# Performance work log

Hardware: AMD Instinct MI355X
Metric: run time of the kernel (lower is better)

Reference implementation:

```python
import jax, jax.numpy as jnp
import numpy as np

OUT_SIZE, EMB, DEC_H, ENC_D = 172, 128, 256, 256
B, L = 256, 1024


def setup_inputs() -> dict:
    key = jax.random.key(0)
    ks = jax.random.split(key, 16)
    s = lambda k, shp, scale=0.05: (jax.random.normal(k, shp, dtype=jnp.float32) * scale)
    return {
        "h0": jax.random.normal(ks[0], (B, DEC_H), dtype=jnp.float32),
        "c0": jax.random.normal(ks[1], (B, DEC_H), dtype=jnp.float32),
        "o_t": jax.random.normal(ks[2], (B, DEC_H), dtype=jnp.float32),
        "enc_out": jax.random.normal(ks[3], (B, L, ENC_D), dtype=jnp.float32),
        "lasttarget": jax.random.randint(ks[4], (B, 1), 0, OUT_SIZE),
        # learned params
        "emb": s(ks[5], (OUT_SIZE, EMB), 1.0),
        "W_ih": s(ks[6], (4 * DEC_H, DEC_H + EMB)),
        "W_hh": s(ks[7], (4 * DEC_H, DEC_H)),
        "b_ih": s(ks[8], (4 * DEC_H,)),
        "b_hh": s(ks[9], (4 * DEC_H,)),
        "W1": s(ks[10], (ENC_D, ENC_D)),
        "W2": s(ks[11], (ENC_D, DEC_H)),
        "W3": s(ks[12], (DEC_H, DEC_H + ENC_D)),
        "W_out": s(ks[13], (OUT_SIZE, DEC_H)),
        "beta": jax.random.uniform(ks[14], (ENC_D,), dtype=jnp.float32, minval=-0.01, maxval=0.01),
    }


def reference(h0, c0, o_t, enc_out, lasttarget, emb, W_ih, W_hh, b_ih, b_hh, W1, W2, W3, W_out, beta):
    # embedding + concat -> LSTMCell input (B, DEC_H+EMB)
    prev_y = emb[lasttarget[:, 0]]              # (B, EMB)
    inp = jnp.concatenate([prev_y, o_t], axis=1)
    # LSTMCell: gate order i, f, g, o (PyTorch convention)
    gates = inp @ W_ih.T + b_ih + h0 @ W_hh.T + b_hh   # (B, 4*DEC_H)
    i, f, g, o = jnp.split(gates, 4, axis=1)
    c_t = jax.nn.sigmoid(f) * c0 + jax.nn.sigmoid(i) * jnp.tanh(g)
    h_t = jax.nn.sigmoid(o) * jnp.tanh(c_t)
    # additive attention over enc positions
    alpha = jnp.tanh(enc_out @ W1.T + (h_t @ W2.T)[:, None, :])  # (B, L, ENC_D)
    scores = jnp.sum(beta * alpha, axis=-1)                      # (B, L)
    attn = jax.nn.softmax(scores, axis=-1)
    context = jnp.einsum("bl,bld->bd", attn, enc_out)            # (B, ENC_D)
    # output projection
    o_new = jnp.tanh(jnp.concatenate([h_t, context], axis=1) @ W3.T)  # (B, DEC_H)
    logit = jax.nn.softmax(o_new @ W_out.T, axis=1)                   # (B, OUT_SIZE)
    return (h_t, c_t, o_new, logit)
```

## Files before the change

### kernel.cpp

```cpp
#include <hip/hip_runtime.h>

#define B_   256
#define L_   1024
#define H_   256
#define EMB_ 128
#define OUT_ 172

typedef float f32x4 __attribute__((ext_vector_type(4)));
typedef __bf16 bf16x8 __attribute__((ext_vector_type(8)));
typedef unsigned short us8 __attribute__((ext_vector_type(8)));

static __device__ __forceinline__ unsigned short f2bf(float f) {
    unsigned u = __float_as_uint(f);
    u += 0x7fffu + ((u >> 16) & 1u);
    return (unsigned short)(u >> 16);
}
static __device__ __forceinline__ float bf2f(unsigned short s) {
    return __uint_as_float(((unsigned)s) << 16);
}
static __device__ __forceinline__ us8 cvt8(const float* __restrict__ p) {
    float4 x0 = *(const float4*)p, x1 = *(const float4*)(p + 4);
    us8 v;
    v[0]=f2bf(x0.x); v[1]=f2bf(x0.y); v[2]=f2bf(x0.z); v[3]=f2bf(x0.w);
    v[4]=f2bf(x1.x); v[5]=f2bf(x1.y); v[6]=f2bf(x1.z); v[7]=f2bf(x1.w);
    return v;
}
static __device__ __forceinline__ float tanh_fast(float x) {
    float e = __expf(2.f * x);
    return 1.f - 2.f * __builtin_amdgcn_rcpf(e + 1.f);
}
static __device__ __forceinline__ float sigm_fast(float x) {
    return __builtin_amdgcn_rcpf(1.f + __expf(-x));
}

#define TS 40

__global__ __launch_bounds__(256) void k_gates(
    const float* __restrict__ h0, const float* __restrict__ o_t,
    const int* __restrict__ lasttarget, const float* __restrict__ emb,
    const float* __restrict__ W_ih, const float* __restrict__ W_hh,
    const float* __restrict__ b_ih, const float* __restrict__ b_hh,
    float* __restrict__ gates)
{
    const int m0 = (blockIdx.x >> 4) * 64;
    const int n0 = (blockIdx.x & 15) * 64;
    const int tid = threadIdx.x;
    const int w = tid >> 6, lane = tid & 63, quad = lane >> 4, l15 = lane & 15;

    __shared__ __align__(16) unsigned short As[64 * TS];
    __shared__ __align__(16) unsigned short Bs[64 * TS];

    float bias[4];
    #pragma unroll
    for (int nt = 0; nt < 4; nt++) {
        int n = n0 + nt * 16 + l15;
        bias[nt] = b_ih[n] + b_hh[n];
    }

    f32x4 acc[4] = {{0,0,0,0},{0,0,0,0},{0,0,0,0},{0,0,0,0}};
    const int sm = tid >> 2, sk8 = (tid & 3) * 8;
    const int lt = lasttarget[m0 + sm];

    for (int kc = 0; kc < 20; kc++) {
        const int k = kc * 32 + sk8;
        const float* ap;
        if (k < 128)      ap = emb + lt * EMB_ + k;
        else if (k < 384) ap = o_t + (m0 + sm) * H_ + (k - 128);
        else              ap = h0  + (m0 + sm) * H_ + (k - 384);
        *(us8*)&As[sm * TS + sk8] = cvt8(ap);
        const int j = n0 + sm;
        const float* bp = (k < 384) ? (W_ih + j * 384 + k) : (W_hh + j * 256 + (k - 384));
        *(us8*)&Bs[sm * TS + sk8] = cvt8(bp);
        __syncthreads();
        bf16x8 a = __builtin_bit_cast(bf16x8, *(const us8*)&As[(w * 16 + l15) * TS + quad * 8]);
        #pragma unroll
        for (int nt = 0; nt < 4; nt++) {
            bf16x8 b = __builtin_bit_cast(bf16x8, *(const us8*)&Bs[(nt * 16 + l15) * TS + quad * 8]);
            acc[nt] = __builtin_amdgcn_mfma_f32_16x16x32_bf16(a, b, acc[nt], 0, 0, 0);
        }
        __syncthreads();
    }
    #pragma unroll
    for (int nt = 0; nt < 4; nt++)
        #pragma unroll
        for (int r = 0; r < 4; r++)
            gates[(m0 + w * 16 + quad * 4 + r) * 1024 + n0 + nt * 16 + l15] = acc[nt][r] + bias[nt];
}

__global__ __launch_bounds__(256) void k_lstm(
    const float* __restrict__ gates, const float* __restrict__ c0,
    float* __restrict__ out, unsigned short* __restrict__ A3u)
{
    const int b = blockIdx.x, t = threadIdx.x;
    const float* g = gates + b * 1024;
    float gi = g[t], gf = g[256 + t], gg = g[512 + t], go = g[768 + t];
    float c = sigm_fast(gf) * c0[b * H_ + t] + sigm_fast(gi) * tanh_fast(gg);
    float h = sigm_fast(go) * tanh_fast(c);
    out[b * H_ + t]           = h;
    out[B_ * H_ + b * H_ + t] = c;
    A3u[b * 512 + t] = f2bf(h);
}

__global__ __launch_bounds__(256) void k_hw2(
    const unsigned short* __restrict__ A3u, const float* __restrict__ W2,
    float* __restrict__ hW2)
{
    const int m0 = (blockIdx.x >> 2) * 64;
    const int n0 = (blockIdx.x & 3) * 64;
    const int tid = threadIdx.x;
    const int w = tid >> 6, lane = tid & 63, quad = lane >> 4, l15 = lane & 15;
    __shared__ __align__(16) unsigned short As[64 * TS];
    __shared__ __align__(16) unsigned short Bs[64 * TS];
    f32x4 acc[4] = {{0,0,0,0},{0,0,0,0},{0,0,0,0},{0,0,0,0}};
    const int sm = tid >> 2, sk8 = (tid & 3) * 8;
    for (int kc = 0; kc < 8; kc++) {
        const int k = kc * 32 + sk8;
        *(us8*)&As[sm * TS + sk8] = *(const us8*)&A3u[(m0 + sm) * 512 + k];
        *(us8*)&Bs[sm * TS + sk8] = cvt8(W2 + (n0 + sm) * 256 + k);
        __syncthreads();
        bf16x8 a = __builtin_bit_cast(bf16x8, *(const us8*)&As[(w * 16 + l15) * TS + quad * 8]);
        #pragma unroll
        for (int nt = 0; nt < 4; nt++) {
            bf16x8 b = __builtin_bit_cast(bf16x8, *(const us8*)&Bs[(nt * 16 + l15) * TS + quad * 8]);
            acc[nt] = __builtin_amdgcn_mfma_f32_16x16x32_bf16(a, b, acc[nt], 0, 0, 0);
        }
        __syncthreads();
    }
    #pragma unroll
    for (int nt = 0; nt < 4; nt++)
        #pragma unroll
        for (int r = 0; r < 4; r++)
            hW2[(m0 + w * 16 + quad * 4 + r) * 256 + n0 + nt * 16 + l15] = acc[nt][r];
}

#define ROWSTR 264

__global__ __launch_bounds__(512, 2) void k_attn(
    const float* __restrict__ enc, const float* __restrict__ W1,
    const float* __restrict__ hW2, const float* __restrict__ beta,
    unsigned short* __restrict__ A3u)
{
    const int b = blockIdx.x;
    const int tid = threadIdx.x;
    const int wave = tid >> 6, lane = tid & 63;
    const int quad = lane >> 4, l15 = lane & 15;

    __shared__ __align__(16) unsigned short encs[2][16 * ROWSTR];
    __shared__ float sp[8][16];
    __shared__ float wexp[16];
    __shared__ float2 cr[512];
    __shared__ float ssum_s;

    bf16x8 wf[8][2];
    float hw2v[2], betav[2];
    #pragma unroll
    for (int nt = 0; nt < 2; nt++) {
        int n = wave * 32 + nt * 16 + l15;
        hw2v[nt]  = hW2[b * H_ + n];
        betav[nt] = beta[n];
        #pragma unroll
        for (int ks = 0; ks < 8; ks++)
            wf[ks][nt] = __builtin_bit_cast(bf16x8, cvt8(W1 + n * 256 + ks * 32 + quad * 8));
    }

    const float* encb = enc + (size_t)b * L_ * H_;
    const int srow = tid >> 5, scol = (tid & 31) * 8;

    *(us8*)&encs[0][srow * ROWSTR + scol] = cvt8(encb + srow * 256 + scol);
    __syncthreads();

    const int cp = tid & 127, q = tid >> 7;
    float2 ctx2 = {0.f, 0.f};
    float ssum = 0.f;

    for (int it = 0; it < 64; it++) {
        const int cur = it & 1;
        float4 x0, x1;
        if (it < 63) {
            const float* p = encb + (it + 1) * 16 * 256 + srow * 256 + scol;
            x0 = *(const float4*)p; x1 = *(const float4*)(p + 4);
        }
        f32x4 acc0 = {0,0,0,0}, acc1 = {0,0,0,0};
        const unsigned short* arow = &encs[cur][l15 * ROWSTR + quad * 8];
        #pragma unroll
        for (int ks = 0; ks < 8; ks++) {
            bf16x8 a = __builtin_bit_cast(bf16x8, *(const us8*)(arow + ks * 32));
            acc0 = __builtin_amdgcn_mfma_f32_16x16x32_bf16(a, wf[ks][0], acc0, 0, 0, 0);
            acc1 = __builtin_amdgcn_mfma_f32_16x16x32_bf16(a, wf[ks][1], acc1, 0, 0, 0);
        }
        float p4[4];
        #pragma unroll
        for (int r = 0; r < 4; r++) {
            float t0 = tanh_fast(acc0[r] + hw2v[0]);
            float t1 = tanh_fast(acc1[r] + hw2v[1]);
            p4[r] = betav[0] * t0 + betav[1] * t1;
        }
        #pragma unroll
        for (int m = 1; m < 16; m <<= 1) {
            p4[0] += __shfl_xor(p4[0], m);
            p4[1] += __shfl_xor(p4[1], m);
            p4[2] += __shfl_xor(p4[2], m);
            p4[3] += __shfl_xor(p4[3], m);
        }
        if (l15 == 0) {
            #pragma unroll
            for (int r = 0; r < 4; r++) sp[wave][quad * 4 + r] = p4[r];
        }
        __syncthreads();
        if (tid < 16) {
            float sc = sp[0][tid] + sp[1][tid] + sp[2][tid] + sp[3][tid]
                     + sp[4][tid] + sp[5][tid] + sp[6][tid] + sp[7][tid];
            wexp[tid] = __expf(sc);
        }
        __syncthreads();
        if (it < 63) {
            us8 v;
            v[0]=f2bf(x0.x); v[1]=f2bf(x0.y); v[2]=f2bf(x0.z); v[3]=f2bf(x0.w);
            v[4]=f2bf(x1.x); v[5]=f2bf(x1.y); v[6]=f2bf(x1.z); v[7]=f2bf(x1.w);
            *(us8*)&encs[cur ^ 1][srow * ROWSTR + scol] = v;
        }
        {
            const unsigned* base = (const unsigned*)&encs[cur][0];
            float cx = ctx2.x, cy = ctx2.y;
            #pragma unroll
            for (int r = 0; r < 4; r++) {
                const int row = q * 4 + r;
                unsigned u = base[row * (ROWSTR / 2) + cp];
                float wv = wexp[row];
                cx += wv * __uint_as_float(u << 16);
                cy += wv * __uint_as_float(u & 0xffff0000u);
            }
            ctx2.x = cx; ctx2.y = cy;
        }
        if (tid == 0) {
            float s2 = 0.f;
            #pragma unroll
            for (int r = 0; r < 16; r++) s2 += wexp[r];
            ssum += s2;
        }
        __syncthreads();
    }
    if (tid == 0) ssum_s = ssum;
    cr[tid] = ctx2;
    __syncthreads();
    if (tid < 128) {
        float2 a0 = cr[tid], a1 = cr[tid + 128], a2 = cr[tid + 256], a3 = cr[tid + 384];
        float inv = __builtin_amdgcn_rcpf(ssum_s);
        float cx = (a0.x + a1.x + a2.x + a3.x) * inv;
        float cy = (a0.y + a1.y + a2.y + a3.y) * inv;
        unsigned pack = (unsigned)f2bf(cx) | ((unsigned)f2bf(cy) << 16);
        ((unsigned*)A3u)[b * 256 + 128 + tid] = pack;
    }
}

__global__ __launch_bounds__(256) void k_out3(
    const unsigned short* __restrict__ A3u, const float* __restrict__ W3,
    float* __restrict__ out, unsigned short* __restrict__ A4u)
{
    const int m0 = (blockIdx.x >> 2) * 64;
    const int n0 = (blockIdx.x & 3) * 64;
    const int tid = threadIdx.x;
    const int w = tid >> 6, lane = tid & 63, quad = lane >> 4, l15 = lane & 15;
    __shared__ __align__(16) unsigned short As[64 * TS];
    __shared__ __align__(16) unsigned short Bs[64 * TS];
    f32x4 acc[4] = {{0,0,0,0},{0,0,0,0},{0,0,0,0},{0,0,0,0}};
    const int sm = tid >> 2, sk8 = (tid & 3) * 8;
    for (int kc = 0; kc < 16; kc++) {
        const int k = kc * 32 + sk8;
        *(us8*)&As[sm * TS + sk8] = *(const us8*)&A3u[(m0 + sm) * 512 + k];
        *(us8*)&Bs[sm * TS + sk8] = cvt8(W3 + (n0 + sm) * 512 + k);
        __syncthreads();
        bf16x8 a = __builtin_bit_cast(bf16x8, *(const us8*)&As[(w * 16 + l15) * TS + quad * 8]);
        #pragma unroll
        for (int nt = 0; nt < 4; nt++) {
            bf16x8 b = __builtin_bit_cast(bf16x8, *(const us8*)&Bs[(nt * 16 + l15) * TS + quad * 8]);
            acc[nt] = __builtin_amdgcn_mfma_f32_16x16x32_bf16(a, b, acc[nt], 0, 0, 0);
        }
        __syncthreads();
    }
    #pragma unroll
    for (int nt = 0; nt < 4; nt++)
        #pragma unroll
        for (int r = 0; r < 4; r++) {
            int row = m0 + w * 16 + quad * 4 + r, col = n0 + nt * 16 + l15;
            float o = tanh_fast(acc[nt][r]);
            out[2 * B_ * H_ + row * 256 + col] = o;
            A4u[row * 256 + col] = f2bf(o);
        }
}

__global__ __launch_bounds__(256) void k_logit(
    const unsigned short* __restrict__ A4u, const float* __restrict__ W_out,
    float* __restrict__ out)
{
    const int m0 = blockIdx.x * 64;
    const int tid = threadIdx.x;
    const int w = tid >> 6, lane = tid & 63, quad = lane >> 4, l15 = lane & 15;
    __shared__ __align__(16) unsigned short As[64 * TS];
    __shared__ __align__(16) unsigned short Bs[192 * TS];
    __shared__ float lg[64][196];
    f32x4 acc[12];
    #pragma unroll
    for (int nt = 0; nt < 12; nt++) acc[nt] = (f32x4){0,0,0,0};
    const int sm = tid >> 2, sk8 = (tid & 3) * 8;
    for (int kc = 0; kc < 8; kc++) {
        const int k = kc * 32 + sk8;
        *(us8*)&As[sm * TS + sk8] = *(const us8*)&A4u[(m0 + sm) * 256 + k];
        #pragma unroll
        for (int rr = 0; rr < 3; rr++) {
            int j = rr * 64 + sm;
            us8 v = {0,0,0,0,0,0,0,0};
            if (j < OUT_) v = cvt8(W_out + j * 256 + k);
            *(us8*)&Bs[j * TS + sk8] = v;
        }
        __syncthreads();
        bf16x8 a = __builtin_bit_cast(bf16x8, *(const us8*)&As[(w * 16 + l15) * TS + quad * 8]);
        #pragma unroll
        for (int nt = 0; nt < 12; nt++) {
            bf16x8 b = __builtin_bit_cast(bf16x8, *(const us8*)&Bs[(nt * 16 + l15) * TS + quad * 8]);
            acc[nt] = __builtin_amdgcn_mfma_f32_16x16x32_bf16(a, b, acc[nt], 0, 0, 0);
        }
        __syncthreads();
    }
    #pragma unroll
    for (int nt = 0; nt < 12; nt++)
        #pragma unroll
        for (int r = 0; r < 4; r++)
            lg[w * 16 + quad * 4 + r][nt * 16 + l15] = acc[nt][r];
    __syncthreads();
    const int m = tid >> 2, p = tid & 3;
    const int cb = p * 43;
    float mx = -1e30f;
    for (int c = 0; c < 43; c++) mx = fmaxf(mx, lg[m][cb + c]);
    mx = fmaxf(mx, __shfl_xor(mx, 1));
    mx = fmaxf(mx, __shfl_xor(mx, 2));
    float s = 0.f;
    for (int c = 0; c < 43; c++) { float e = __expf(lg[m][cb + c] - mx); lg[m][cb + c] = e; s += e; }
    s += __shfl_xor(s, 1);
    s += __shfl_xor(s, 2);
    float inv = 1.f / s;
    for (int c = 0; c < 43; c++)
        out[3 * B_ * H_ + (m0 + m) * OUT_ + cb + c] = lg[m][cb + c] * inv;
}

extern "C" void kernel_launch(void* const* d_in, const int* in_sizes, int n_in,
                              void* d_out, int out_size, void* d_ws, size_t ws_size,
                              hipStream_t stream)
{
    const float* h0   = (const float*)d_in[0];
    const float* c0   = (const float*)d_in[1];
    const float* o_t  = (const float*)d_in[2];
    const float* enc  = (const float*)d_in[3];
    const int*   lt   = (const int*)  d_in[4];
    const float* emb  = (const float*)d_in[5];
    const float* W_ih = (const float*)d_in[6];
    const float* W_hh = (const float*)d_in[7];
    const float* b_ih = (const float*)d_in[8];
    const float* b_hh = (const float*)d_in[9];
    const float* W1   = (const float*)d_in[10];
    const float* W2   = (const float*)d_in[11];
    const float* W3   = (const float*)d_in[12];
    const float* Wo   = (const float*)d_in[13];
    const float* beta = (const float*)d_in[14];
    float* out = (float*)d_out;
    float* ws  = (float*)d_ws;

    float*          gates = ws;
    float*          hW2   = ws + 262144;
    unsigned short* A3u   = (unsigned short*)(ws + 327680);
    unsigned short* A4u   = (unsigned short*)(ws + 393216);

    k_gates<<<64, 256, 0, stream>>>(h0, o_t, lt, emb, W_ih, W_hh, b_ih, b_hh, gates);
    k_lstm <<<256, 256, 0, stream>>>(gates, c0, out, A3u);
    k_hw2  <<<16, 256, 0, stream>>>(A3u, W2, hW2);
    k_attn <<<256, 512, 0, stream>>>(enc, W1, hW2, beta, A3u);
    k_out3 <<<16, 256, 0, stream>>>(A3u, W3, out, A4u);
    k_logit<<<4, 256, 0, stream>>>(A4u, Wo, out);
}
```

Measured before the change: 466.1 us.

## Split attention over two blocks per batch row with triple-buffered pipeline

The attention kernel now runs two blocks per batch element, each covering half the sequence and writing partial context sums and exp-sums to workspace. The output projection kernel combines the two partials, normalizes and converts to bf16 as it loads its A tile. The attention loop moves to a three-slot LDS ring with loads issued two tiles ahead and double-buffered score arrays, which removes one barrier per iteration. The goal is better occupancy across 256 CUs and less synchronization stall, at the cost of an extra partial-buffer round trip and more LDS per block.

```diff
diff --git a/kernel.cpp b/kernel.cpp
--- a/kernel.cpp
+++ b/kernel.cpp
@@ -98,7 +98,7 @@
     float h = sigm_fast(go) * tanh_fast(c);
     out[b * H_ + t]           = h;
     out[B_ * H_ + b * H_ + t] = c;
-    A3u[b * 512 + t] = f2bf(h);
+    A3u[b * 256 + t] = f2bf(h);
 }
 
 __global__ __launch_bounds__(256) void k_hw2(
@@ -115,7 +115,7 @@
     const int sm = tid >> 2, sk8 = (tid & 3) * 8;
     for (int kc = 0; kc < 8; kc++) {
         const int k = kc * 32 + sk8;
-        *(us8*)&As[sm * TS + sk8] = *(const us8*)&A3u[(m0 + sm) * 512 + k];
+        *(us8*)&As[sm * TS + sk8] = *(const us8*)&A3u[(m0 + sm) * 256 + k];
         *(us8*)&Bs[sm * TS + sk8] = cvt8(W2 + (n0 + sm) * 256 + k);
         __syncthreads();
         bf16x8 a = __builtin_bit_cast(bf16x8, *(const us8*)&As[(w * 16 + l15) * TS + quad * 8]);
@@ -138,18 +138,18 @@
 __global__ __launch_bounds__(512, 2) void k_attn(
     const float* __restrict__ enc, const float* __restrict__ W1,
     const float* __restrict__ hW2, const float* __restrict__ beta,
-    unsigned short* __restrict__ A3u)
-{
-    const int b = blockIdx.x;
+    float* __restrict__ ctx_part, float* __restrict__ s_part)
+{
+    const int blk = blockIdx.x;
+    const int b = blk >> 1, half = blk & 1;
     const int tid = threadIdx.x;
     const int wave = tid >> 6, lane = tid & 63;
     const int quad = lane >> 4, l15 = lane & 15;
 
-    __shared__ __align__(16) unsigned short encs[2][16 * ROWSTR];
-    __shared__ float sp[8][16];
-    __shared__ float wexp[16];
+    __shared__ __align__(16) unsigned short encs[3][16 * ROWSTR];
+    __shared__ float sp[2][8][16];
+    __shared__ float wexp[2][16];
     __shared__ float2 cr[512];
-    __shared__ float ssum_s;
 
     bf16x8 wf[8][2];
     float hw2v[2], betav[2];
@@ -163,22 +163,29 @@
             wf[ks][nt] = __builtin_bit_cast(bf16x8, cvt8(W1 + n * 256 + ks * 32 + quad * 8));
     }
 
-    const float* encb = enc + (size_t)b * L_ * H_;
+    const float* encb = enc + ((size_t)b * L_ + half * 512) * H_;
     const int srow = tid >> 5, scol = (tid & 31) * 8;
 
     *(us8*)&encs[0][srow * ROWSTR + scol] = cvt8(encb + srow * 256 + scol);
+    float4 x0, x1;
+    {
+        const float* p = encb + 16 * 256 + srow * 256 + scol;
+        x0 = *(const float4*)p; x1 = *(const float4*)(p + 4);
+    }
     __syncthreads();
 
     const int cp = tid & 127, q = tid >> 7;
     float2 ctx2 = {0.f, 0.f};
     float ssum = 0.f;
 
-    for (int it = 0; it < 64; it++) {
-        const int cur = it & 1;
-        float4 x0, x1;
-        if (it < 63) {
-            const float* p = encb + (it + 1) * 16 * 256 + srow * 256 + scol;
-            x0 = *(const float4*)p; x1 = *(const float4*)(p + 4);
+    for (int it = 0; it < 32; it++) {
+        const int cur = it % 3;
+        const int nxt = (it + 1) % 3;
+        const int par = it & 1;
+        float4 y0 = {0,0,0,0}, y1 = {0,0,0,0};
+        if (it < 30) {
+            const float* p = encb + (it + 2) * 16 * 256 + srow * 256 + scol;
+            y0 = *(const float4*)p; y1 = *(const float4*)(p + 4);
         }
         f32x4 acc0 = {0,0,0,0}, acc1 = {0,0,0,0};
         const unsigned short* arow = &encs[cur][l15 * ROWSTR + quad * 8];
@@ -187,6 +194,12 @@
             bf16x8 a = __builtin_bit_cast(bf16x8, *(const us8*)(arow + ks * 32));
             acc0 = __builtin_amdgcn_mfma_f32_16x16x32_bf16(a, wf[ks][0], acc0, 0, 0, 0);
             acc1 = __builtin_amdgcn_mfma_f32_16x16x32_bf16(a, wf[ks][1], acc1, 0, 0, 0);
+        }
+        if (it < 31) {
+            us8 v;
+            v[0]=f2bf(x0.x); v[1]=f2bf(x0.y); v[2]=f2bf(x0.z); v[3]=f2bf(x0.w);
+            v[4]=f2bf(x1.x); v[5]=f2bf(x1.y); v[6]=f2bf(x1.z); v[7]=f2bf(x1.w);
+            *(us8*)&encs[nxt][srow * ROWSTR + scol] = v;
         }
         float p4[4];
         #pragma unroll
@@ -204,21 +217,15 @@
         }
         if (l15 == 0) {
             #pragma unroll
-            for (int r = 0; r < 4; r++) sp[wave][quad * 4 + r] = p4[r];
+            for (int r = 0; r < 4; r++) sp[par][wave][quad * 4 + r] = p4[r];
         }
         __syncthreads();
         if (tid < 16) {
-            float sc = sp[0][tid] + sp[1][tid] + sp[2][tid] + sp[3][tid]
-                     + sp[4][tid] + sp[5][tid] + sp[6][tid] + sp[7][tid];
-            wexp[tid] = __expf(sc);
-        }
-        __syncthreads();
-        if (it < 63) {
-            us8 v;
-            v[0]=f2bf(x0.x); v[1]=f2bf(x0.y); v[2]=f2bf(x0.z); v[3]=f2bf(x0.w);
-            v[4]=f2bf(x1.x); v[5]=f2bf(x1.y); v[6]=f2bf(x1.z); v[7]=f2bf(x1.w);
-            *(us8*)&encs[cur ^ 1][srow * ROWSTR + scol] = v;
-        }
+            float sc = sp[par][0][tid] + sp[par][1][tid] + sp[par][2][tid] + sp[par][3][tid]
+                     + sp[par][4][tid] + sp[par][5][tid] + sp[par][6][tid] + sp[par][7][tid];
+            wexp[par][tid] = __expf(sc);
+        }
+        __syncthreads();
         {
             const unsigned* base = (const unsigned*)&encs[cur][0];
             float cx = ctx2.x, cy = ctx2.y;
@@ -226,7 +233,7 @@
             for (int r = 0; r < 4; r++) {
                 const int row = q * 4 + r;
                 unsigned u = base[row * (ROWSTR / 2) + cp];
-                float wv = wexp[row];
+                float wv = wexp[par][row];
                 cx += wv * __uint_as_float(u << 16);
                 cy += wv * __uint_as_float(u & 0xffff0000u);
             }
@@ -235,26 +242,26 @@
         if (tid == 0) {
             float s2 = 0.f;
             #pragma unroll
-            for (int r = 0; r < 16; r++) s2 += wexp[r];
+            for (int r = 0; r < 16; r++) s2 += wexp[par][r];
             ssum += s2;
         }
-        __syncthreads();
-    }
-    if (tid == 0) ssum_s = ssum;
+        x0 = y0; x1 = y1;
+    }
     cr[tid] = ctx2;
     __syncthreads();
+    if (tid == 0) s_part[blk] = ssum;
     if (tid < 128) {
         float2 a0 = cr[tid], a1 = cr[tid + 128], a2 = cr[tid + 256], a3 = cr[tid + 384];
-        float inv = __builtin_amdgcn_rcpf(ssum_s);
-        float cx = (a0.x + a1.x + a2.x + a3.x) * inv;
-        float cy = (a0.y + a1.y + a2.y + a3.y) * inv;
-        unsigned pack = (unsigned)f2bf(cx) | ((unsigned)f2bf(cy) << 16);
-        ((unsigned*)A3u)[b * 256 + 128 + tid] = pack;
+        float2 o;
+        o.x = a0.x + a1.x + a2.x + a3.x;
+        o.y = a0.y + a1.y + a2.y + a3.y;
+        ((float2*)ctx_part)[blk * 128 + tid] = o;
     }
 }
 
 __global__ __launch_bounds__(256) void k_out3(
-    const unsigned short* __restrict__ A3u, const float* __restrict__ W3,
+    const unsigned short* __restrict__ A3u, const float* __restrict__ ctx_part,
+    const float* __restrict__ s_part, const float* __restrict__ W3,
     float* __restrict__ out, unsigned short* __restrict__ A4u)
 {
     const int m0 = (blockIdx.x >> 2) * 64;
@@ -265,9 +272,25 @@
     __shared__ __align__(16) unsigned short Bs[64 * TS];
     f32x4 acc[4] = {{0,0,0,0},{0,0,0,0},{0,0,0,0},{0,0,0,0}};
     const int sm = tid >> 2, sk8 = (tid & 3) * 8;
+    const int bb = m0 + sm;
+    const float inv = 1.f / (s_part[2 * bb] + s_part[2 * bb + 1]);
     for (int kc = 0; kc < 16; kc++) {
         const int k = kc * 32 + sk8;
-        *(us8*)&As[sm * TS + sk8] = *(const us8*)&A3u[(m0 + sm) * 512 + k];
+        if (k < 256) {
+            *(us8*)&As[sm * TS + sk8] = *(const us8*)&A3u[bb * 256 + k];
+        } else {
+            const int c = k - 256;
+            const float* p0 = ctx_part + (size_t)(2 * bb) * 256 + c;
+            const float* p1 = ctx_part + (size_t)(2 * bb + 1) * 256 + c;
+            float4 a0 = *(const float4*)p0, a1 = *(const float4*)(p0 + 4);
+            float4 b0 = *(const float4*)p1, b1 = *(const float4*)(p1 + 4);
+            us8 v;
+            v[0]=f2bf((a0.x+b0.x)*inv); v[1]=f2bf((a0.y+b0.y)*inv);
+            v[2]=f2bf((a0.z+b0.z)*inv); v[3]=f2bf((a0.w+b0.w)*inv);
+            v[4]=f2bf((a1.x+b1.x)*inv); v[5]=f2bf((a1.y+b1.y)*inv);
+            v[6]=f2bf((a1.z+b1.z)*inv); v[7]=f2bf((a1.w+b1.w)*inv);
+            *(us8*)&As[sm * TS + sk8] = v;
+        }
         *(us8*)&Bs[sm * TS + sk8] = cvt8(W3 + (n0 + sm) * 512 + k);
         __syncthreads();
         bf16x8 a = __builtin_bit_cast(bf16x8, *(const us8*)&As[(w * 16 + l15) * TS + quad * 8]);
@@ -365,15 +388,17 @@
     float* out = (float*)d_out;
     float* ws  = (float*)d_ws;
 
-    float*          gates = ws;
-    float*          hW2   = ws + 262144;
-    unsigned short* A3u   = (unsigned short*)(ws + 327680);
-    unsigned short* A4u   = (unsigned short*)(ws + 393216);
+    float*          gates    = ws;
+    float*          hW2      = ws + 262144;
+    float*          ctx_part = ws + 327680;
+    float*          s_part   = ws + 458752;
+    unsigned short* A3u      = (unsigned short*)(ws + 459264);
+    unsigned short* A4u      = (unsigned short*)(ws + 492032);
 
     k_gates<<<64, 256, 0, stream>>>(h0, o_t, lt, emb, W_ih, W_hh, b_ih, b_hh, gates);
     k_lstm <<<256, 256, 0, stream>>>(gates, c0, out, A3u);
     k_hw2  <<<16, 256, 0, stream>>>(A3u, W2, hW2);
-    k_attn <<<256, 512, 0, stream>>>(enc, W1, hW2, beta, A3u);
-    k_out3 <<<16, 256, 0, stream>>>(A3u, W3, out, A4u);
+    k_attn <<<512, 512, 0, stream>>>(enc, W1, hW2, beta, ctx_part, s_part);
+    k_out3 <<<16, 256, 0, stream>>>(A3u, ctx_part, s_part, W3, out, A4u);
     k_logit<<<4, 256, 0, stream>>>(A4u, Wo, out);
 }
```

Measured after the change: 464.1 us. No clear change (-0.4%).

## Fuse gates, LSTM, hW2 and attention into one cooperative kernel with triple buffering

Applied to the files above, without the earlier changes.

Merges the gate GEMM, LSTM cell, h·W2 projection and attention kernels into a single cooperative launch. A grid-wide sync separates the gate GEMM (done by the first 64 blocks) from the per-batch work, and the first two encoder tiles are prefetched before that sync. Each block then computes its own h·W2 row in shared memory. The attention loop moves from double to triple buffering with parity-indexed score arrays, so the bf16 store of the next tile overlaps the current MFMAs and one barrier per iteration is dropped. This removes three launches and the hW2 round trip through global memory. In exchange it relies on cooperative launch residency (256 blocks of 512 threads) and repeats the W2 load in every block.

```diff
diff --git a/kernel.cpp b/kernel.cpp
--- a/kernel.cpp
+++ b/kernel.cpp
@@ -1,4 +1,5 @@
 #include <hip/hip_runtime.h>
+#include <hip/hip_cooperative_groups.h>
 
 #define B_   256
 #define L_   1024
@@ -14,9 +15,6 @@
     unsigned u = __float_as_uint(f);
     u += 0x7fffu + ((u >> 16) & 1u);
     return (unsigned short)(u >> 16);
-}
-static __device__ __forceinline__ float bf2f(unsigned short s) {
-    return __uint_as_float(((unsigned)s) << 16);
 }
 static __device__ __forceinline__ us8 cvt8(const float* __restrict__ p) {
     float4 x0 = *(const float4*)p, x1 = *(const float4*)(p + 4);
@@ -25,6 +23,12 @@
     v[4]=f2bf(x1.x); v[5]=f2bf(x1.y); v[6]=f2bf(x1.z); v[7]=f2bf(x1.w);
     return v;
 }
+static __device__ __forceinline__ us8 cvt8r(float4 x0, float4 x1) {
+    us8 v;
+    v[0]=f2bf(x0.x); v[1]=f2bf(x0.y); v[2]=f2bf(x0.z); v[3]=f2bf(x0.w);
+    v[4]=f2bf(x1.x); v[5]=f2bf(x1.y); v[6]=f2bf(x1.z); v[7]=f2bf(x1.w);
+    return v;
+}
 static __device__ __forceinline__ float tanh_fast(float x) {
     float e = __expf(2.f * x);
     return 1.f - 2.f * __builtin_amdgcn_rcpf(e + 1.f);
@@ -34,160 +38,156 @@
 }
 
 #define TS 40
-
-__global__ __launch_bounds__(256) void k_gates(
-    const float* __restrict__ h0, const float* __restrict__ o_t,
-    const int* __restrict__ lasttarget, const float* __restrict__ emb,
+#define ROWSTR 264
+
+__global__ __launch_bounds__(512, 2) void k_fused(
+    const float* __restrict__ h0, const float* __restrict__ c0,
+    const float* __restrict__ o_t, const float* __restrict__ enc,
+    const int* __restrict__ lt, const float* __restrict__ emb,
     const float* __restrict__ W_ih, const float* __restrict__ W_hh,
     const float* __restrict__ b_ih, const float* __restrict__ b_hh,
-    float* __restrict__ gates)
+    const float* __restrict__ W1, const float* __restrict__ W2,
+    const float* __restrict__ beta, float* __restrict__ gates,
+    unsigned short* __restrict__ A3u, float* __restrict__ out)
 {
-    const int m0 = (blockIdx.x >> 4) * 64;
-    const int n0 = (blockIdx.x & 15) * 64;
-    const int tid = threadIdx.x;
-    const int w = tid >> 6, lane = tid & 63, quad = lane >> 4, l15 = lane & 15;
-
-    __shared__ __align__(16) unsigned short As[64 * TS];
-    __shared__ __align__(16) unsigned short Bs[64 * TS];
-
-    float bias[4];
-    #pragma unroll
-    for (int nt = 0; nt < 4; nt++) {
-        int n = n0 + nt * 16 + l15;
-        bias[nt] = b_ih[n] + b_hh[n];
-    }
-
-    f32x4 acc[4] = {{0,0,0,0},{0,0,0,0},{0,0,0,0},{0,0,0,0}};
-    const int sm = tid >> 2, sk8 = (tid & 3) * 8;
-    const int lt = lasttarget[m0 + sm];
-
-    for (int kc = 0; kc < 20; kc++) {
-        const int k = kc * 32 + sk8;
-        const float* ap;
-        if (k < 128)      ap = emb + lt * EMB_ + k;
-        else if (k < 384) ap = o_t + (m0 + sm) * H_ + (k - 128);
-        else              ap = h0  + (m0 + sm) * H_ + (k - 384);
-        *(us8*)&As[sm * TS + sk8] = cvt8(ap);
-        const int j = n0 + sm;
-        const float* bp = (k < 384) ? (W_ih + j * 384 + k) : (W_hh + j * 256 + (k - 384));
-        *(us8*)&Bs[sm * TS + sk8] = cvt8(bp);
-        __syncthreads();
-        bf16x8 a = __builtin_bit_cast(bf16x8, *(const us8*)&As[(w * 16 + l15) * TS + quad * 8]);
-        #pragma unroll
-        for (int nt = 0; nt < 4; nt++) {
-            bf16x8 b = __builtin_bit_cast(bf16x8, *(const us8*)&Bs[(nt * 16 + l15) * TS + quad * 8]);
-            acc[nt] = __builtin_amdgcn_mfma_f32_16x16x32_bf16(a, b, acc[nt], 0, 0, 0);
-        }
-        __syncthreads();
-    }
-    #pragma unroll
-    for (int nt = 0; nt < 4; nt++)
-        #pragma unroll
-        for (int r = 0; r < 4; r++)
-            gates[(m0 + w * 16 + quad * 4 + r) * 1024 + n0 + nt * 16 + l15] = acc[nt][r] + bias[nt];
-}
-
-__global__ __launch_bounds__(256) void k_lstm(
-    const float* __restrict__ gates, const float* __restrict__ c0,
-    float* __restrict__ out, unsigned short* __restrict__ A3u)
-{
-    const int b = blockIdx.x, t = threadIdx.x;
-    const float* g = gates + b * 1024;
-    float gi = g[t], gf = g[256 + t], gg = g[512 + t], go = g[768 + t];
-    float c = sigm_fast(gf) * c0[b * H_ + t] + sigm_fast(gi) * tanh_fast(gg);
-    float h = sigm_fast(go) * tanh_fast(c);
-    out[b * H_ + t]           = h;
-    out[B_ * H_ + b * H_ + t] = c;
-    A3u[b * 512 + t] = f2bf(h);
-}
-
-__global__ __launch_bounds__(256) void k_hw2(
-    const unsigned short* __restrict__ A3u, const float* __restrict__ W2,
-    float* __restrict__ hW2)
-{
-    const int m0 = (blockIdx.x >> 2) * 64;
-    const int n0 = (blockIdx.x & 3) * 64;
-    const int tid = threadIdx.x;
-    const int w = tid >> 6, lane = tid & 63, quad = lane >> 4, l15 = lane & 15;
-    __shared__ __align__(16) unsigned short As[64 * TS];
-    __shared__ __align__(16) unsigned short Bs[64 * TS];
-    f32x4 acc[4] = {{0,0,0,0},{0,0,0,0},{0,0,0,0},{0,0,0,0}};
-    const int sm = tid >> 2, sk8 = (tid & 3) * 8;
-    for (int kc = 0; kc < 8; kc++) {
-        const int k = kc * 32 + sk8;
-        *(us8*)&As[sm * TS + sk8] = *(const us8*)&A3u[(m0 + sm) * 512 + k];
-        *(us8*)&Bs[sm * TS + sk8] = cvt8(W2 + (n0 + sm) * 256 + k);
-        __syncthreads();
-        bf16x8 a = __builtin_bit_cast(bf16x8, *(const us8*)&As[(w * 16 + l15) * TS + quad * 8]);
-        #pragma unroll
-        for (int nt = 0; nt < 4; nt++) {
-            bf16x8 b = __builtin_bit_cast(bf16x8, *(const us8*)&Bs[(nt * 16 + l15) * TS + quad * 8]);
-            acc[nt] = __builtin_amdgcn_mfma_f32_16x16x32_bf16(a, b, acc[nt], 0, 0, 0);
-        }
-        __syncthreads();
-    }
-    #pragma unroll
-    for (int nt = 0; nt < 4; nt++)
-        #pragma unroll
-        for (int r = 0; r < 4; r++)
-            hW2[(m0 + w * 16 + quad * 4 + r) * 256 + n0 + nt * 16 + l15] = acc[nt][r];
-}
-
-#define ROWSTR 264
-
-__global__ __launch_bounds__(512, 2) void k_attn(
-    const float* __restrict__ enc, const float* __restrict__ W1,
-    const float* __restrict__ hW2, const float* __restrict__ beta,
-    unsigned short* __restrict__ A3u)
-{
-    const int b = blockIdx.x;
+    const int blk = blockIdx.x;
     const int tid = threadIdx.x;
     const int wave = tid >> 6, lane = tid & 63;
     const int quad = lane >> 4, l15 = lane & 15;
 
-    __shared__ __align__(16) unsigned short encs[2][16 * ROWSTR];
-    __shared__ float sp[8][16];
-    __shared__ float wexp[16];
+    __shared__ __align__(16) union {
+        struct { unsigned short As[64 * TS]; unsigned short Bs[64 * TS]; } g;
+        unsigned short encs[3][16 * ROWSTR];
+        float W2c[256 * 33];
+    } su;
+    __shared__ float h_s[256];
+    __shared__ float hw2p[512];
+    __shared__ float hw2_s[256];
+    __shared__ float sp[2][8][16];
+    __shared__ float wexp[2][16];
     __shared__ float2 cr[512];
     __shared__ float ssum_s;
+
+    if (blk < 64) {
+        const int m0 = (blk >> 4) * 64, n0 = (blk & 15) * 64;
+        const int mh = (wave & 1) * 32, nq = (wave >> 1) * 16;
+        f32x4 acc[2] = {{0,0,0,0},{0,0,0,0}};
+        const int st = tid & 255, sm = st >> 2, sk8 = (st & 3) * 8;
+        int ltv = 0;
+        if (tid < 256) ltv = lt[m0 + sm];
+        for (int kc = 0; kc < 20; kc++) {
+            const int k = kc * 32 + sk8;
+            if (tid < 256) {
+                const float* ap;
+                if (k < 128)      ap = emb + ltv * EMB_ + k;
+                else if (k < 384) ap = o_t + (m0 + sm) * H_ + (k - 128);
+                else              ap = h0  + (m0 + sm) * H_ + (k - 384);
+                *(us8*)&su.g.As[sm * TS + sk8] = cvt8(ap);
+            } else {
+                const int j = n0 + sm;
+                const float* bp = (k < 384) ? (W_ih + j * 384 + k)
+                                            : (W_hh + j * 256 + (k - 384));
+                *(us8*)&su.g.Bs[sm * TS + sk8] = cvt8(bp);
+            }
+            __syncthreads();
+            bf16x8 bfr = __builtin_bit_cast(bf16x8, *(const us8*)&su.g.Bs[(nq + l15) * TS + quad * 8]);
+            #pragma unroll
+            for (int mf = 0; mf < 2; mf++) {
+                bf16x8 a = __builtin_bit_cast(bf16x8, *(const us8*)&su.g.As[(mh + mf * 16 + l15) * TS + quad * 8]);
+                acc[mf] = __builtin_amdgcn_mfma_f32_16x16x32_bf16(a, bfr, acc[mf], 0, 0, 0);
+            }
+            __syncthreads();
+        }
+        const int n = n0 + nq + l15;
+        const float bias = b_ih[n] + b_hh[n];
+        #pragma unroll
+        for (int mf = 0; mf < 2; mf++)
+            #pragma unroll
+            for (int r = 0; r < 4; r++)
+                gates[(m0 + mh + mf * 16 + quad * 4 + r) * 1024 + n] = acc[mf][r] + bias;
+    }
+
+    const float* encb = enc + (size_t)blk * L_ * H_;
+    const int srow = tid >> 5, scol = (tid & 31) * 8;
+    float4 x0, x1, y0, y1;
+    { const float* p = encb + srow * 256 + scol;        x0 = *(const float4*)p; x1 = *(const float4*)(p + 4); }
+    { const float* p = encb + 4096 + srow * 256 + scol; y0 = *(const float4*)p; y1 = *(const float4*)(p + 4); }
+
+    cooperative_groups::this_grid().sync();
+
+    const int b = blk;
+    if (tid < 256) {
+        const float* g = gates + b * 1024;
+        float gi = g[tid], gf = g[256 + tid], gg = g[512 + tid], go = g[768 + tid];
+        float c = sigm_fast(gf) * c0[b * H_ + tid] + sigm_fast(gi) * tanh_fast(gg);
+        float h = sigm_fast(go) * tanh_fast(c);
+        out[b * H_ + tid]           = h;
+        out[B_ * H_ + b * H_ + tid] = c;
+        A3u[b * 512 + tid] = f2bf(h);
+        h_s[tid] = h;
+    }
+    float hacc = 0.f;
+    const int t2 = tid & 255, jb = (tid >> 8) * 16;
+    for (int kc = 0; kc < 8; kc++) {
+        __syncthreads();
+        {
+            const int rr = tid >> 1, cb = (tid & 1) * 16;
+            const float* wp = W2 + rr * 256 + kc * 32 + cb;
+            float4 w0 = *(const float4*)wp, w1 = *(const float4*)(wp + 4);
+            float4 w2v = *(const float4*)(wp + 8), w3v = *(const float4*)(wp + 12);
+            float* d = &su.W2c[rr * 33 + cb];
+            d[0]=w0.x; d[1]=w0.y; d[2]=w0.z; d[3]=w0.w;
+            d[4]=w1.x; d[5]=w1.y; d[6]=w1.z; d[7]=w1.w;
+            d[8]=w2v.x; d[9]=w2v.y; d[10]=w2v.z; d[11]=w2v.w;
+            d[12]=w3v.x; d[13]=w3v.y; d[14]=w3v.z; d[15]=w3v.w;
+        }
+        __syncthreads();
+        #pragma unroll
+        for (int j = 0; j < 16; j++)
+            hacc += h_s[kc * 32 + jb + j] * su.W2c[t2 * 33 + jb + j];
+    }
+    hw2p[tid] = hacc;
+    __syncthreads();
+    if (tid < 256) hw2_s[tid] = hw2p[tid] + hw2p[tid + 256];
+    *(us8*)&su.encs[0][srow * ROWSTR + scol] = cvt8r(x0, x1);
+    x0 = y0; x1 = y1;
+    __syncthreads();
 
     bf16x8 wf[8][2];
     float hw2v[2], betav[2];
     #pragma unroll
     for (int nt = 0; nt < 2; nt++) {
         int n = wave * 32 + nt * 16 + l15;
-        hw2v[nt]  = hW2[b * H_ + n];
+        hw2v[nt]  = hw2_s[n];
         betav[nt] = beta[n];
         #pragma unroll
         for (int ks = 0; ks < 8; ks++)
             wf[ks][nt] = __builtin_bit_cast(bf16x8, cvt8(W1 + n * 256 + ks * 32 + quad * 8));
     }
-
-    const float* encb = enc + (size_t)b * L_ * H_;
-    const int srow = tid >> 5, scol = (tid & 31) * 8;
-
-    *(us8*)&encs[0][srow * ROWSTR + scol] = cvt8(encb + srow * 256 + scol);
-    __syncthreads();
 
     const int cp = tid & 127, q = tid >> 7;
     float2 ctx2 = {0.f, 0.f};
     float ssum = 0.f;
 
     for (int it = 0; it < 64; it++) {
-        const int cur = it & 1;
-        float4 x0, x1;
-        if (it < 63) {
-            const float* p = encb + (it + 1) * 16 * 256 + srow * 256 + scol;
-            x0 = *(const float4*)p; x1 = *(const float4*)(p + 4);
+        const int cur = it % 3;
+        const int nxt = (it + 1) % 3;
+        const int par = it & 1;
+        float4 yy0 = {0,0,0,0}, yy1 = {0,0,0,0};
+        if (it < 62) {
+            const float* p = encb + (it + 2) * 4096 + srow * 256 + scol;
+            yy0 = *(const float4*)p; yy1 = *(const float4*)(p + 4);
         }
         f32x4 acc0 = {0,0,0,0}, acc1 = {0,0,0,0};
-        const unsigned short* arow = &encs[cur][l15 * ROWSTR + quad * 8];
+        const unsigned short* arow = &su.encs[cur][l15 * ROWSTR + quad * 8];
         #pragma unroll
         for (int ks = 0; ks < 8; ks++) {
             bf16x8 a = __builtin_bit_cast(bf16x8, *(const us8*)(arow + ks * 32));
             acc0 = __builtin_amdgcn_mfma_f32_16x16x32_bf16(a, wf[ks][0], acc0, 0, 0, 0);
             acc1 = __builtin_amdgcn_mfma_f32_16x16x32_bf16(a, wf[ks][1], acc1, 0, 0, 0);
         }
+        if (it < 63)
+            *(us8*)&su.encs[nxt][srow * ROWSTR + scol] = cvt8r(x0, x1);
         float p4[4];
         #pragma unroll
         for (int r = 0; r < 4; r++) {
@@ -204,29 +204,23 @@
         }
         if (l15 == 0) {
             #pragma unroll
-            for (int r = 0; r < 4; r++) sp[wave][quad * 4 + r] = p4[r];
+            for (int r = 0; r < 4; r++) sp[par][wave][quad * 4 + r] = p4[r];
         }
         __syncthreads();
         if (tid < 16) {
-            float sc = sp[0][tid] + sp[1][tid] + sp[2][tid] + sp[3][tid]
-                     + sp[4][tid] + sp[5][tid] + sp[6][tid] + sp[7][tid];
-            wexp[tid] = __expf(sc);
-        }
-        __syncthreads();
-        if (it < 63) {
-            us8 v;
-            v[0]=f2bf(x0.x); v[1]=f2bf(x0.y); v[2]=f2bf(x0.z); v[3]=f2bf(x0.w);
-            v[4]=f2bf(x1.x); v[5]=f2bf(x1.y); v[6]=f2bf(x1.z); v[7]=f2bf(x1.w);
-            *(us8*)&encs[cur ^ 1][srow * ROWSTR + scol] = v;
-        }
+            float sc = sp[par][0][tid] + sp[par][1][tid] + sp[par][2][tid] + sp[par][3][tid]
+                     + sp[par][4][tid] + sp[par][5][tid] + sp[par][6][tid] + sp[par][7][tid];
+            wexp[par][tid] = __expf(sc);
+        }
+        __syncthreads();
         {
-            const unsigned* base = (const unsigned*)&encs[cur][0];
+            const unsigned* base = (const unsigned*)&su.encs[cur][0];
             float cx = ctx2.x, cy = ctx2.y;
             #pragma unroll
             for (int r = 0; r < 4; r++) {
                 const int row = q * 4 + r;
                 unsigned u = base[row * (ROWSTR / 2) + cp];
-                float wv = wexp[row];
+                float wv = wexp[par][row];
                 cx += wv * __uint_as_float(u << 16);
                 cy += wv * __uint_as_float(u & 0xffff0000u);
             }
@@ -235,9 +229,10 @@
         if (tid == 0) {
             float s2 = 0.f;
             #pragma unroll
-            for (int r = 0; r < 16; r++) s2 += wexp[r];
+            for (int r = 0; r < 16; r++) s2 += wexp[par][r];
             ssum += s2;
         }
+        x0 = yy0; x1 = yy1;
         __syncthreads();
     }
     if (tid == 0) ssum_s = ssum;
@@ -273,8 +268,8 @@
         bf16x8 a = __builtin_bit_cast(bf16x8, *(const us8*)&As[(w * 16 + l15) * TS + quad * 8]);
         #pragma unroll
         for (int nt = 0; nt < 4; nt++) {
-            bf16x8 b = __builtin_bit_cast(bf16x8, *(const us8*)&Bs[(nt * 16 + l15) * TS + quad * 8]);
-            acc[nt] = __builtin_amdgcn_mfma_f32_16x16x32_bf16(a, b, acc[nt], 0, 0, 0);
+            bf16x8 bfr = __builtin_bit_cast(bf16x8, *(const us8*)&Bs[(nt * 16 + l15) * TS + quad * 8]);
+            acc[nt] = __builtin_amdgcn_mfma_f32_16x16x32_bf16(a, bfr, acc[nt], 0, 0, 0);
         }
         __syncthreads();
     }
@@ -317,8 +312,8 @@
         bf16x8 a = __builtin_bit_cast(bf16x8, *(const us8*)&As[(w * 16 + l15) * TS + quad * 8]);
         #pragma unroll
         for (int nt = 0; nt < 12; nt++) {
-            bf16x8 b = __builtin_bit_cast(bf16x8, *(const us8*)&Bs[(nt * 16 + l15) * TS + quad * 8]);
-            acc[nt] = __builtin_amdgcn_mfma_f32_16x16x32_bf16(a, b, acc[nt], 0, 0, 0);
+            bf16x8 bfr = __builtin_bit_cast(bf16x8, *(const us8*)&Bs[(nt * 16 + l15) * TS + quad * 8]);
+            acc[nt] = __builtin_amdgcn_mfma_f32_16x16x32_bf16(a, bfr, acc[nt], 0, 0, 0);
         }
         __syncthreads();
     }
@@ -366,14 +361,15 @@
     float* ws  = (float*)d_ws;
 
     float*          gates = ws;
-    float*          hW2   = ws + 262144;
-    unsigned short* A3u   = (unsigned short*)(ws + 327680);
-    unsigned short* A4u   = (unsigned short*)(ws + 393216);
-
-    k_gates<<<64, 256, 0, stream>>>(h0, o_t, lt, emb, W_ih, W_hh, b_ih, b_hh, gates);
-    k_lstm <<<256, 256, 0, stream>>>(gates, c0, out, A3u);
-    k_hw2  <<<16, 256, 0, stream>>>(A3u, W2, hW2);
-    k_attn <<<256, 512, 0, stream>>>(enc, W1, hW2, beta, A3u);
+    unsigned short* A3u   = (unsigned short*)(ws + 262144);
+    unsigned short* A4u   = (unsigned short*)(ws + 262144 + 65536);
+
+    void* args[] = { (void*)&h0, (void*)&c0, (void*)&o_t, (void*)&enc, (void*)&lt,
+                     (void*)&emb, (void*)&W_ih, (void*)&W_hh, (void*)&b_ih, (void*)&b_hh,
+                     (void*)&W1, (void*)&W2, (void*)&beta,
+                     (void*)&gates, (void*)&A3u, (void*)&out };
+    hipLaunchCooperativeKernel((const void*)k_fused, dim3(256), dim3(512), args, 0, stream);
+
     k_out3 <<<16, 256, 0, stream>>>(A3u, W3, out, A4u);
     k_logit<<<4, 256, 0, stream>>>(A4u, Wo, out);
 }
```

After: 513.8 us. +10.2%, slower.
